# Performance work log

Measured on AMD Instinct MI355X. Metric: run time of the kernel, lower is better.

## Reference

```python
import jax, jax.numpy as jnp
import numpy as np

DT = 0.01
B, K, T_LEN = 1024, 256, 256


def setup_inputs() -> dict:
    key = jax.random.key(0)
    k1, k2, k3 = jax.random.split(key, 3)
    x = jax.random.normal(k1, (B, K), dtype=jnp.float32)
    # small init so exp(mu*dt) stays near 1 over a 256-step rollout
    W1 = jax.random.normal(k2, (K, K), dtype=jnp.float32) * 0.02
    b1 = jnp.zeros((K,), dtype=jnp.float32)
    W2 = jax.random.normal(k3, (K, K), dtype=jnp.float32) * 0.02
    b2 = jnp.zeros((K,), dtype=jnp.float32)
    return {"x": x, "W1": W1, "b1": b1, "W2": W2, "b2": b2, "T": T_LEN}


def reference(x, W1, b1, W2, b2, T):
    batch, k = x.shape
    ne = k // 2  # num_eigenvalues
    # parameterization MLP: Linear -> tanh -> Linear
    h = jnp.tanh(x @ W1 + b1)
    eigs = (h @ W2 + b2).reshape(batch, ne, 2)
    mu = eigs[..., 0]
    omega = eigs[..., 1]
    exp_mu = jnp.exp(mu * DT)
    a = exp_mu * jnp.cos(omega * DT)  # diagonal of 2x2 rotation-scaling
    b = exp_mu * jnp.sin(omega * DT)  # off-diagonal

    def step(z, _):
        zp = z.reshape(batch, ne, 2)
        z0 = a * zp[..., 0] - b * zp[..., 1]
        z1 = b * zp[..., 0] + a * zp[..., 1]
        zn = jnp.stack([z0, z1], axis=-1).reshape(batch, k)
        return zn, zn

    _, preds = jax.lax.scan(step, x, None, length=T)  # [T, B, K]
    return jnp.transpose(preds, (1, 0, 2))  # [B, T, K]
```

## Files before the change

kernel.cpp:

```cpp
#include <hip/hip_runtime.h>


#define DT_CONST 0.01f

typedef float f32x4 __attribute__((ext_vector_type(4)));

constexpr int KDIM  = 256;
constexpr int KHALF = 128;
constexpr int AROWS = 4;

__global__ __launch_bounds__(512, 4) void koopman_fused(
    const float* __restrict__ x,  const float* __restrict__ W1,
    const float* __restrict__ b1, const float* __restrict__ W2,
    const float* __restrict__ b2, float* __restrict__ out, int T)
{
    __shared__ alignas(16) float part[2][AROWS][KDIM];
    __shared__ alignas(16) float hs[AROWS][KDIM];
    __shared__ alignas(16) float coef[AROWS][KDIM];

    const int tid = threadIdx.x;
    const int j   = tid & (KDIM - 1);
    const int kh  = tid >> 8;
    const int b0  = blockIdx.x * AROWS;

    float acc[AROWS];

    {
#pragma unroll
        for (int r = 0; r < AROWS; ++r) acc[r] = 0.f;
        const float* xb = x + (size_t)b0 * KDIM + kh * KHALF;
        const float* w  = W1 + (size_t)kh * KHALF * KDIM + j;
#pragma unroll 8
        for (int k = 0; k < KHALF; ++k) {
            float wk = w[(size_t)k * KDIM];
#pragma unroll
            for (int r = 0; r < AROWS; ++r)
                acc[r] = fmaf(xb[r * KDIM + k], wk, acc[r]);
        }
#pragma unroll
        for (int r = 0; r < AROWS; ++r) part[kh][r][j] = acc[r];
    }
    __syncthreads();
    if (kh == 0) {
#pragma unroll
        for (int r = 0; r < AROWS; ++r)
            hs[r][j] = tanhf(part[0][r][j] + part[1][r][j] + b1[j]);
    }
    __syncthreads();

    {
#pragma unroll
        for (int r = 0; r < AROWS; ++r) acc[r] = 0.f;
        const float* w = W2 + (size_t)kh * KHALF * KDIM + j;
#pragma unroll 2
        for (int k4 = 0; k4 < KHALF / 4; ++k4) {
            f32x4 hv[AROWS];
#pragma unroll
            for (int r = 0; r < AROWS; ++r)
                hv[r] = *reinterpret_cast<const f32x4*>(&hs[r][kh * KHALF + k4 * 4]);
#pragma unroll
            for (int i = 0; i < 4; ++i) {
                float wk = w[(size_t)(k4 * 4 + i) * KDIM];
#pragma unroll
                for (int r = 0; r < AROWS; ++r)
                    acc[r] = fmaf(hv[r][i], wk, acc[r]);
            }
        }
#pragma unroll
        for (int r = 0; r < AROWS; ++r) part[kh][r][j] = acc[r];
    }
    __syncthreads();
    if (kh == 0) {
#pragma unroll
        for (int r = 0; r < AROWS; ++r)
            coef[r][j] = (part[0][r][j] + part[1][r][j] + b2[j]) * DT_CONST;
    }
    __syncthreads();

    const int wave = tid >> 6;
    const int lane = tid & 63;
    const int r    = wave & (AROWS - 1);
    const int tseg = wave >> 2;
    const int b    = b0 + r;
    const int tlen = (T + 1) >> 1;
    const int t0   = tseg * tlen;

    const f32x4 c  = *reinterpret_cast<const f32x4*>(&coef[r][lane * 4]);
    const f32x4 xv = *reinterpret_cast<const f32x4*>(x + (size_t)b * KDIM + lane * 4);

    const float tf = (float)t0;
    float s, co, e;
    e = expf(c.x * tf); sincosf(c.y * tf, &s, &co);
    float z0 = e * (co * xv.x - s * xv.y);
    float z1 = e * (s * xv.x + co * xv.y);
    e = expf(c.z * tf); sincosf(c.w * tf, &s, &co);
    float z2 = e * (co * xv.z - s * xv.w);
    float z3 = e * (s * xv.z + co * xv.w);

    e = expf(c.x); sincosf(c.y, &s, &co);
    const float a0 = e * co, g0 = e * s;
    e = expf(c.z); sincosf(c.w, &s, &co);
    const float a1 = e * co, g1 = e * s;

    f32x4* orow = reinterpret_cast<f32x4*>(out + ((size_t)b * T + t0) * KDIM) + lane;
    const int nt = ((t0 + tlen < T) ? tlen : (T - t0));
#pragma unroll 4
    for (int t = 0; t < nt; ++t) {
        float n0 = a0 * z0 - g0 * z1;
        float n1 = g0 * z0 + a0 * z1;
        float n2 = a1 * z2 - g1 * z3;
        float n3 = g1 * z2 + a1 * z3;
        f32x4 v = { n0, n1, n2, n3 };
        *orow = v;
        orow += KDIM / 4;
        z0 = n0; z1 = n1; z2 = n2; z3 = n3;
    }
}

extern "C" void kernel_launch(void* const* d_in, const int* in_sizes, int n_in,
                              void* d_out, int out_size, void* d_ws, size_t ws_size,
                              hipStream_t stream) {
    const float* x  = (const float*)d_in[0];
    const float* W1 = (const float*)d_in[1];
    const float* b1 = (const float*)d_in[2];
    const float* W2 = (const float*)d_in[3];
    const float* b2 = (const float*)d_in[4];

    const int Kd = in_sizes[2];
    const int Bb = in_sizes[0] / Kd;
    const int T  = out_size / (Bb * Kd);

    float* out = (float*)d_out;

    koopman_fused<<<Bb / AROWS, 512, 0, stream>>>(x, W1, b1, W2, b2, out, T);
}
```

Baseline: 61.37 us.

## Stage MLP weights into LDS with double-buffered async global_load_lds chunks

The two matvec stages now copy W1 and W2 into shared memory 32 rows at a time using global_load_lds, double-buffered so the next chunk loads while the current one is consumed. x is also staged once into LDS and reused for the rollout's initial state. This targets the strided, uncoalesced per-thread global weight reads. In exchange the kernel uses about 80KB of LDS per block, which lowers occupancy, and adds a block barrier per chunk. The output-write loop that likely dominates runtime is unchanged.

```diff
diff --git a/kernel.cpp b/kernel.cpp
--- a/kernel.cpp
+++ b/kernel.cpp
@@ -5,70 +5,117 @@
 
 typedef float f32x4 __attribute__((ext_vector_type(4)));
 
-constexpr int KDIM  = 256;
-constexpr int KHALF = 128;
-constexpr int AROWS = 4;
+constexpr int KDIM   = 256;
+constexpr int AROWS  = 4;
+constexpr int CROWS  = 32;
+constexpr int NCHUNK = KDIM / CROWS;
+constexpr int NW     = 8;
+constexpr int RPW    = CROWS / NW;
 
-__global__ __launch_bounds__(512, 4) void koopman_fused(
+__device__ __forceinline__ void stage_row(const float* gsrc, float* ldst, int lane)
+{
+    __builtin_amdgcn_global_load_lds(
+        (const __attribute__((address_space(1))) void*)(gsrc + lane * 4),
+        (__attribute__((address_space(3))) void*)ldst,
+        16, 0, 0);
+}
+
+__device__ __forceinline__ void stage_chunk(const float* W, int c, float* buf,
+                                            int wave, int lane)
+{
+#pragma unroll
+    for (int i = 0; i < RPW; ++i) {
+        const int row = wave * RPW + i;
+        stage_row(W + (size_t)(c * CROWS + row) * KDIM, buf + row * KDIM, lane);
+    }
+}
+
+__global__ __launch_bounds__(512) void koopman_fused(
     const float* __restrict__ x,  const float* __restrict__ W1,
     const float* __restrict__ b1, const float* __restrict__ W2,
     const float* __restrict__ b2, float* __restrict__ out, int T)
 {
-    __shared__ alignas(16) float part[2][AROWS][KDIM];
+    __shared__ alignas(16) float Wb[2][CROWS * KDIM];
+    __shared__ alignas(16) float xs[AROWS][KDIM];
     __shared__ alignas(16) float hs[AROWS][KDIM];
     __shared__ alignas(16) float coef[AROWS][KDIM];
+    __shared__ alignas(16) float part[2][AROWS][KDIM];
 
-    const int tid = threadIdx.x;
-    const int j   = tid & (KDIM - 1);
-    const int kh  = tid >> 8;
-    const int b0  = blockIdx.x * AROWS;
+    const int tid  = threadIdx.x;
+    const int j    = tid & (KDIM - 1);
+    const int kh   = tid >> 8;
+    const int wave = tid >> 6;
+    const int lane = tid & 63;
+    const int b0   = blockIdx.x * AROWS;
+
+    for (int i = tid; i < AROWS * KDIM; i += 512)
+        xs[i >> 8][i & (KDIM - 1)] = x[(size_t)b0 * KDIM + i];
+    stage_chunk(W1, 0, Wb[0], wave, lane);
+    __syncthreads();
 
     float acc[AROWS];
 
-    {
 #pragma unroll
-        for (int r = 0; r < AROWS; ++r) acc[r] = 0.f;
-        const float* xb = x + (size_t)b0 * KDIM + kh * KHALF;
-        const float* w  = W1 + (size_t)kh * KHALF * KDIM + j;
-#pragma unroll 8
-        for (int k = 0; k < KHALF; ++k) {
-            float wk = w[(size_t)k * KDIM];
+    for (int r = 0; r < AROWS; ++r) acc[r] = 0.f;
+    for (int c = 0; c < NCHUNK; ++c) {
+        const int cur = c & 1;
+        if (c + 1 < NCHUNK)
+            stage_chunk(W1, c + 1, Wb[cur ^ 1], wave, lane);
+#pragma unroll
+        for (int g = 0; g < 4; ++g) {
+            const int kl = kh * 16 + g * 4;
+            const int kg = c * CROWS + kl;
+            f32x4 xv[AROWS];
 #pragma unroll
             for (int r = 0; r < AROWS; ++r)
-                acc[r] = fmaf(xb[r * KDIM + k], wk, acc[r]);
+                xv[r] = *reinterpret_cast<const f32x4*>(&xs[r][kg]);
+#pragma unroll
+            for (int i = 0; i < 4; ++i) {
+                const float wk = Wb[cur][(kl + i) * KDIM + j];
+#pragma unroll
+                for (int r = 0; r < AROWS; ++r)
+                    acc[r] = fmaf(xv[r][i], wk, acc[r]);
+            }
         }
+        __syncthreads();
+    }
 #pragma unroll
-        for (int r = 0; r < AROWS; ++r) part[kh][r][j] = acc[r];
-    }
+    for (int r = 0; r < AROWS; ++r) part[kh][r][j] = acc[r];
     __syncthreads();
     if (kh == 0) {
 #pragma unroll
         for (int r = 0; r < AROWS; ++r)
             hs[r][j] = tanhf(part[0][r][j] + part[1][r][j] + b1[j]);
     }
+    stage_chunk(W2, 0, Wb[0], wave, lane);
     __syncthreads();
 
-    {
 #pragma unroll
-        for (int r = 0; r < AROWS; ++r) acc[r] = 0.f;
-        const float* w = W2 + (size_t)kh * KHALF * KDIM + j;
-#pragma unroll 2
-        for (int k4 = 0; k4 < KHALF / 4; ++k4) {
+    for (int r = 0; r < AROWS; ++r) acc[r] = 0.f;
+    for (int c = 0; c < NCHUNK; ++c) {
+        const int cur = c & 1;
+        if (c + 1 < NCHUNK)
+            stage_chunk(W2, c + 1, Wb[cur ^ 1], wave, lane);
+#pragma unroll
+        for (int g = 0; g < 4; ++g) {
+            const int kl = kh * 16 + g * 4;
+            const int kg = c * CROWS + kl;
             f32x4 hv[AROWS];
 #pragma unroll
             for (int r = 0; r < AROWS; ++r)
-                hv[r] = *reinterpret_cast<const f32x4*>(&hs[r][kh * KHALF + k4 * 4]);
+                hv[r] = *reinterpret_cast<const f32x4*>(&hs[r][kg]);
 #pragma unroll
             for (int i = 0; i < 4; ++i) {
-                float wk = w[(size_t)(k4 * 4 + i) * KDIM];
+                const float wk = Wb[cur][(kl + i) * KDIM + j];
 #pragma unroll
                 for (int r = 0; r < AROWS; ++r)
                     acc[r] = fmaf(hv[r][i], wk, acc[r]);
             }
         }
+        __syncthreads();
+    }
 #pragma unroll
-        for (int r = 0; r < AROWS; ++r) part[kh][r][j] = acc[r];
-    }
+    for (int r = 0; r < AROWS; ++r) part[kh][r][j] = acc[r];
     __syncthreads();
     if (kh == 0) {
 #pragma unroll
@@ -77,8 +124,6 @@
     }
     __syncthreads();
 
-    const int wave = tid >> 6;
-    const int lane = tid & 63;
     const int r    = wave & (AROWS - 1);
     const int tseg = wave >> 2;
     const int b    = b0 + r;
@@ -86,7 +131,7 @@
     const int t0   = tseg * tlen;
 
     const f32x4 c  = *reinterpret_cast<const f32x4*>(&coef[r][lane * 4]);
-    const f32x4 xv = *reinterpret_cast<const f32x4*>(x + (size_t)b * KDIM + lane * 4);
+    const f32x4 xv = *reinterpret_cast<const f32x4*>(&xs[r][lane * 4]);
 
     const float tf = (float)t0;
     float s, co, e;
```

Measured after the change: 62.63 us. 2.0% more time.

## Split MLP matvecs into 8 K-slices with float4 weight loads and staged x

Applied to the files above, without the earlier changes.

Restructures both MLP matvec phases so each wave handles a 32-wide K slice and each lane computes four adjacent output columns using float4 weight loads, instead of a two-way K split with scalar per-column loads. The input rows are staged once in shared memory and reused by the matvec and the rollout initialisation. The bias-add and tanh reductions are spread across all threads rather than half the block. Shared-memory use grows (the partial-sum buffer is four times larger), the min-blocks launch bound is dropped, and the reduction now sums eight partials per output.

```diff
diff --git a/kernel.cpp b/kernel.cpp
--- a/kernel.cpp
+++ b/kernel.cpp
@@ -5,75 +5,100 @@
 
 typedef float f32x4 __attribute__((ext_vector_type(4)));
 
-constexpr int KDIM  = 256;
-constexpr int KHALF = 128;
-constexpr int AROWS = 4;
+constexpr int KDIM   = 256;
+constexpr int AROWS  = 4;
+constexpr int KSPLIT = 8;
+constexpr int KSLICE = KDIM / KSPLIT;
 
-__global__ __launch_bounds__(512, 4) void koopman_fused(
+__global__ __launch_bounds__(512) void koopman_fused(
     const float* __restrict__ x,  const float* __restrict__ W1,
     const float* __restrict__ b1, const float* __restrict__ W2,
     const float* __restrict__ b2, float* __restrict__ out, int T)
 {
-    __shared__ alignas(16) float part[2][AROWS][KDIM];
+    __shared__ alignas(16) float xs[AROWS][KDIM];
     __shared__ alignas(16) float hs[AROWS][KDIM];
     __shared__ alignas(16) float coef[AROWS][KDIM];
+    __shared__ alignas(16) float part[KSPLIT][AROWS][KDIM];
 
     const int tid = threadIdx.x;
-    const int j   = tid & (KDIM - 1);
-    const int kh  = tid >> 8;
+    const int jg  = tid & 63;
+    const int ks  = tid >> 6;
     const int b0  = blockIdx.x * AROWS;
 
-    float acc[AROWS];
+    {
+        const f32x4* xg = reinterpret_cast<const f32x4*>(x + (size_t)b0 * KDIM);
+        f32x4* xl = reinterpret_cast<f32x4*>(&xs[0][0]);
+        for (int i = tid; i < AROWS * KDIM / 4; i += 512) xl[i] = xg[i];
+    }
+    __syncthreads();
+
+    f32x4 acc[AROWS];
 
     {
 #pragma unroll
-        for (int r = 0; r < AROWS; ++r) acc[r] = 0.f;
-        const float* xb = x + (size_t)b0 * KDIM + kh * KHALF;
-        const float* w  = W1 + (size_t)kh * KHALF * KDIM + j;
-#pragma unroll 8
-        for (int k = 0; k < KHALF; ++k) {
-            float wk = w[(size_t)k * KDIM];
+        for (int r = 0; r < AROWS; ++r) acc[r] = (f32x4){0.f, 0.f, 0.f, 0.f};
+        const float* wbase = W1 + (size_t)ks * KSLICE * KDIM + jg * 4;
+#pragma unroll 2
+        for (int k4 = 0; k4 < KSLICE / 4; ++k4) {
+            f32x4 wv[4];
+#pragma unroll
+            for (int i = 0; i < 4; ++i)
+                wv[i] = *reinterpret_cast<const f32x4*>(wbase + (size_t)(k4 * 4 + i) * KDIM);
+            f32x4 xv[AROWS];
 #pragma unroll
             for (int r = 0; r < AROWS; ++r)
-                acc[r] = fmaf(xb[r * KDIM + k], wk, acc[r]);
+                xv[r] = *reinterpret_cast<const f32x4*>(&xs[r][ks * KSLICE + k4 * 4]);
+#pragma unroll
+            for (int i = 0; i < 4; ++i)
+#pragma unroll
+                for (int r = 0; r < AROWS; ++r)
+                    acc[r] += wv[i] * xv[r][i];
         }
 #pragma unroll
-        for (int r = 0; r < AROWS; ++r) part[kh][r][j] = acc[r];
+        for (int r = 0; r < AROWS; ++r)
+            *reinterpret_cast<f32x4*>(&part[ks][r][jg * 4]) = acc[r];
     }
     __syncthreads();
-    if (kh == 0) {
+    for (int idx = tid; idx < AROWS * KDIM; idx += 512) {
+        const int r = idx >> 8, j = idx & (KDIM - 1);
+        float ssum = b1[j];
 #pragma unroll
-        for (int r = 0; r < AROWS; ++r)
-            hs[r][j] = tanhf(part[0][r][j] + part[1][r][j] + b1[j]);
+        for (int s = 0; s < KSPLIT; ++s) ssum += part[s][r][j];
+        hs[r][j] = tanhf(ssum);
     }
     __syncthreads();
 
     {
 #pragma unroll
-        for (int r = 0; r < AROWS; ++r) acc[r] = 0.f;
-        const float* w = W2 + (size_t)kh * KHALF * KDIM + j;
+        for (int r = 0; r < AROWS; ++r) acc[r] = (f32x4){0.f, 0.f, 0.f, 0.f};
+        const float* wbase = W2 + (size_t)ks * KSLICE * KDIM + jg * 4;
 #pragma unroll 2
-        for (int k4 = 0; k4 < KHALF / 4; ++k4) {
+        for (int k4 = 0; k4 < KSLICE / 4; ++k4) {
+            f32x4 wv[4];
+#pragma unroll
+            for (int i = 0; i < 4; ++i)
+                wv[i] = *reinterpret_cast<const f32x4*>(wbase + (size_t)(k4 * 4 + i) * KDIM);
             f32x4 hv[AROWS];
 #pragma unroll
             for (int r = 0; r < AROWS; ++r)
-                hv[r] = *reinterpret_cast<const f32x4*>(&hs[r][kh * KHALF + k4 * 4]);
+                hv[r] = *reinterpret_cast<const f32x4*>(&hs[r][ks * KSLICE + k4 * 4]);
 #pragma unroll
-            for (int i = 0; i < 4; ++i) {
-                float wk = w[(size_t)(k4 * 4 + i) * KDIM];
+            for (int i = 0; i < 4; ++i)
 #pragma unroll
                 for (int r = 0; r < AROWS; ++r)
-                    acc[r] = fmaf(hv[r][i], wk, acc[r]);
-            }
+                    acc[r] += wv[i] * hv[r][i];
         }
 #pragma unroll
-        for (int r = 0; r < AROWS; ++r) part[kh][r][j] = acc[r];
+        for (int r = 0; r < AROWS; ++r)
+            *reinterpret_cast<f32x4*>(&part[ks][r][jg * 4]) = acc[r];
     }
     __syncthreads();
-    if (kh == 0) {
+    for (int idx = tid; idx < AROWS * KDIM; idx += 512) {
+        const int r = idx >> 8, j = idx & (KDIM - 1);
+        float ssum = b2[j];
 #pragma unroll
-        for (int r = 0; r < AROWS; ++r)
-            coef[r][j] = (part[0][r][j] + part[1][r][j] + b2[j]) * DT_CONST;
+        for (int s = 0; s < KSPLIT; ++s) ssum += part[s][r][j];
+        coef[r][j] = ssum * DT_CONST;
     }
     __syncthreads();
 
@@ -86,7 +111,7 @@
     const int t0   = tseg * tlen;
 
     const f32x4 c  = *reinterpret_cast<const f32x4*>(&coef[r][lane * 4]);
-    const f32x4 xv = *reinterpret_cast<const f32x4*>(x + (size_t)b * KDIM + lane * 4);
+    const f32x4 xv = *reinterpret_cast<const f32x4*>(&xs[r][lane * 4]);
 
     const float tf = (float)t0;
     float s, co, e;
```

Result: faster. 52.42 us (-14.6%).
